# Kernel tuning notes

Hardware: AMD Instinct MI355X
Metric: run time of the kernel (lower is better)

The kernel has to match this reference:

```python
import jax, jax.numpy as jnp
import numpy as np

N, M_DIM, CTRL = 16384, 512, 1024
EPS = 1e-16

def setup_inputs() -> dict:
    key = jax.random.key(0)
    k1, k2, k3, k4, k5 = jax.random.split(key, 5)
    embeddings = jax.random.normal(k1, (1, CTRL), dtype=jnp.float32)
    w_prev = jax.random.uniform(k2, (1, N), dtype=jnp.float32)
    w_prev = w_prev / jnp.sum(w_prev, axis=1, keepdims=True)  # valid soft address
    memory = jax.random.normal(k3, (N, M_DIM), dtype=jnp.float32) * 0.05
    out_f = 3 * M_DIM + 6  # write_lengths = [M,1,1,3,1,M,M]
    W = jax.random.normal(k4, (out_f, CTRL), dtype=jnp.float32) * (1.0 / np.sqrt(CTRL))
    b = jax.random.normal(k5, (out_f,), dtype=jnp.float32) * 0.01
    return {"embeddings": embeddings, "w_prev": w_prev, "memory": memory, "W": W, "b": b}

def reference(embeddings, w_prev, memory, W, b):
    Md = memory.shape[1]
    o = (embeddings @ W.T + b).reshape(1, -1)  # [1, 3M+6]
    # column split per write_lengths [M,1,1,3,1,M,M]
    k = o[:, :Md]
    beta = jax.nn.softplus(o[:, Md:Md + 1])
    g = jax.nn.sigmoid(o[:, Md + 1:Md + 2])
    s = jax.nn.softmax(o[:, Md + 2:Md + 5], axis=1)       # 3 circular shifts
    gamma = 1.0 + jax.nn.softplus(o[:, Md + 5:Md + 6])
    e = o[:, Md + 6:2 * Md + 6]                            # erase vector [1,M]
    a = o[:, 2 * Md + 6:]                                  # add vector   [1,M]
    # content addressing: cosine similarity of k against each memory row
    mem_norm = jnp.linalg.norm(memory, axis=1)             # [N]
    k_norm = jnp.linalg.norm(k, axis=1)                    # [1]
    sim = (k @ memory.T) / (k_norm[:, None] * mem_norm[None, :] + EPS)  # [1,N]
    wc = jax.nn.softmax(beta * sim, axis=1)
    # interpolation with previous weights
    wg = g * wc + (1.0 - g) * w_prev
    # circular convolution with 3-tap shift kernel (shifts -1,0,+1)
    ws = (s[:, 0:1] * jnp.roll(wg, 1, axis=1)
          + s[:, 1:2] * wg
          + s[:, 2:3] * jnp.roll(wg, -1, axis=1))
    # sharpening
    wp = jnp.power(ws + EPS, gamma)
    w = wp / jnp.sum(wp, axis=1, keepdims=True)            # [1,N]
    # erase/add outer-product memory write
    erase = w.T @ e                                        # [N,M]
    add = w.T @ a                                          # [N,M]
    new_memory = memory * (1.0 - erase) + add
    return w, new_memory
```

## Files before the change

kernel.cpp:

```cpp
#include <hip/hip_runtime.h>
#include <math.h>

#define N 16384
#define MD 512
#define CTRLDIM 1024
#define OUTF 1542


__device__ __forceinline__ float softplus_f(float x) {
    return (x > 20.f) ? x : log1pf(expf(x));
}

__device__ __forceinline__ float wave_bfly_sum(float v) {
    #pragma unroll
    for (int off = 1; off < 64; off <<= 1) v += __shfl_xor(v, off, 64);
    return v;
}

__global__ void k_proj(const float* __restrict__ emb, const float* __restrict__ W,
                       const float* __restrict__ b, float* __restrict__ O,
                       float* __restrict__ E, float* __restrict__ A) {
    int row = blockIdx.x;
    int t = threadIdx.x;
    const float4* w4 = (const float4*)(W + (size_t)row * CTRLDIM);
    const float4* e4 = (const float4*)emb;
    float4 wv = w4[t];
    float4 ev = e4[t];
    float p = wv.x * ev.x + wv.y * ev.y + wv.z * ev.z + wv.w * ev.w;
    #pragma unroll
    for (int off = 32; off; off >>= 1) p += __shfl_down(p, off, 64);
    __shared__ float s[4];
    int lane = t & 63, wid = t >> 6;
    if (lane == 0) s[wid] = p;
    __syncthreads();
    if (t == 0) {
        float val = s[0] + s[1] + s[2] + s[3] + b[row];
        O[row] = val;
        if (row >= MD + 6 && row < 2 * MD + 6)      E[row - (MD + 6)] = val;
        else if (row >= 2 * MD + 6)                 A[row - (2 * MD + 6)] = val;
    }
}

__global__ void __launch_bounds__(256) k_sim(const float* __restrict__ mem,
                                             const float* __restrict__ O,
                                             float* __restrict__ EZ,
                                             float* __restrict__ PART1) {
    int t = threadIdx.x, lane = t & 63, wid = t >> 6;
    int waveId = blockIdx.x * 4 + wid;
    const float4* k4 = (const float4*)O;
    float4 k0 = k4[lane], k1 = k4[lane + 64];
    float ksq = k0.x * k0.x + k0.y * k0.y + k0.z * k0.z + k0.w * k0.w
              + k1.x * k1.x + k1.y * k1.y + k1.z * k1.z + k1.w * k1.w;
    ksq = wave_bfly_sum(ksq);
    float knorm = sqrtf(ksq);
    float beta = softplus_f(O[MD]);
    int row0 = waveId * 4;
    float4 m0[4], m1[4];
    #pragma unroll
    for (int r = 0; r < 4; r++) {
        const float4* m4 = (const float4*)(mem + (size_t)(row0 + r) * MD);
        m0[r] = m4[lane];
        m1[r] = m4[lane + 64];
    }
    float wsum = 0.f;
    #pragma unroll
    for (int r = 0; r < 4; r++) {
        float dot = m0[r].x * k0.x + m0[r].y * k0.y + m0[r].z * k0.z + m0[r].w * k0.w
                  + m1[r].x * k1.x + m1[r].y * k1.y + m1[r].z * k1.z + m1[r].w * k1.w;
        float nsq = m0[r].x * m0[r].x + m0[r].y * m0[r].y + m0[r].z * m0[r].z + m0[r].w * m0[r].w
                  + m1[r].x * m1[r].x + m1[r].y * m1[r].y + m1[r].z * m1[r].z + m1[r].w * m1[r].w;
        dot = wave_bfly_sum(dot);
        nsq = wave_bfly_sum(nsq);
        float z = beta * dot / (knorm * sqrtf(nsq) + 1e-16f);
        float ez = expf(z - beta);
        if (lane == 0) EZ[row0 + r] = ez;
        wsum += ez;
    }
    __shared__ float sblk[4];
    if (lane == 0) sblk[wid] = wsum;
    __syncthreads();
    if (t == 0) PART1[blockIdx.x] = sblk[0] + sblk[1] + sblk[2] + sblk[3];
}

__global__ void __launch_bounds__(256) k_shift(const float* __restrict__ EZ,
                                               const float* __restrict__ wprev,
                                               const float* __restrict__ O,
                                               const float* __restrict__ PART1,
                                               float* __restrict__ WP,
                                               float* __restrict__ PART2) {
    int t = threadIdx.x, lane = t & 63, wid = t >> 6;
    float v = 0.f;
    #pragma unroll
    for (int j = 0; j < 16; j++) v += PART1[lane + j * 64];
    float inv1 = 1.f / wave_bfly_sum(v);
    float g = 1.f / (1.f + expf(-O[MD + 1]));
    float s0r = O[MD + 2], s1r = O[MD + 3], s2r = O[MD + 4];
    float m = fmaxf(s0r, fmaxf(s1r, s2r));
    float e0 = expf(s0r - m), e1 = expf(s1r - m), e2 = expf(s2r - m);
    float inv_se = 1.f / (e0 + e1 + e2);
    float s0 = e0 * inv_se, s1 = e1 * inv_se, s2 = e2 * inv_se;
    float gamma = 1.f + softplus_f(O[MD + 5]);
    float gm1 = 1.f - g;
    int i = blockIdx.x * 256 + t;
    int im = (i == 0) ? (N - 1) : (i - 1);
    int ip = (i == N - 1) ? 0 : (i + 1);
    float wgm = g * EZ[im] * inv1 + gm1 * wprev[im];
    float wgc = g * EZ[i]  * inv1 + gm1 * wprev[i];
    float wgp = g * EZ[ip] * inv1 + gm1 * wprev[ip];
    float wsv = s0 * wgm + s1 * wgc + s2 * wgp;
    float wp = exp2f(gamma * log2f(wsv + 1e-16f));
    WP[i] = wp;
    float bs = wave_bfly_sum(wp);
    __shared__ float sblk[4];
    if (lane == 0) sblk[wid] = bs;
    __syncthreads();
    if (t == 0) PART2[blockIdx.x] = sblk[0] + sblk[1] + sblk[2] + sblk[3];
}

__global__ void __launch_bounds__(256) k_upd(const float* __restrict__ mem,
                                             const float* __restrict__ WP,
                                             const float* __restrict__ PART2,
                                             const float* __restrict__ E,
                                             const float* __restrict__ A,
                                             float* __restrict__ wout,
                                             float* __restrict__ outMem) {
    int t = threadIdx.x, lane = t & 63;
    float inv2 = 1.f / wave_bfly_sum(PART2[lane]);
    int idx = blockIdx.x * 256 + t;
    int i = idx >> 7;
    int c = idx & 127;
    float wi = WP[i] * inv2;
    if (c == 0) wout[i] = wi;
    float4 m = ((const float4*)mem)[idx];
    float4 e = ((const float4*)E)[c];
    float4 a = ((const float4*)A)[c];
    float4 o;
    o.x = m.x * (1.f - wi * e.x) + wi * a.x;
    o.y = m.y * (1.f - wi * e.y) + wi * a.y;
    o.z = m.z * (1.f - wi * e.z) + wi * a.z;
    o.w = m.w * (1.f - wi * e.w) + wi * a.w;
    ((float4*)outMem)[idx] = o;
}

extern "C" void kernel_launch(void* const* d_in, const int* in_sizes, int n_in,
                              void* d_out, int out_size, void* d_ws, size_t ws_size,
                              hipStream_t stream) {
    const float* emb   = (const float*)d_in[0];
    const float* wprev = (const float*)d_in[1];
    const float* mem   = (const float*)d_in[2];
    const float* W     = (const float*)d_in[3];
    const float* b     = (const float*)d_in[4];
    float* out = (float*)d_out;
    float* wsf = (float*)d_ws;
    float* O     = wsf;
    float* E     = wsf + 1552;
    float* A     = wsf + 2064;
    float* PART1 = wsf + 2576;
    float* PART2 = wsf + 3600;
    float* EZ    = wsf + 3664;
    float* WP    = wsf + 20048;

    k_proj<<<OUTF, 256, 0, stream>>>(emb, W, b, O, E, A);
    k_sim<<<N / 16, 256, 0, stream>>>(mem, O, EZ, PART1);
    k_shift<<<N / 256, 256, 0, stream>>>(EZ, wprev, O, PART1, WP, PART2);
    k_upd<<<(N * (MD / 4)) / 256, 256, 0, stream>>>(mem, WP, PART2, E, A, out, out + N);
}
```

Before: 110.9 us.

## Fuse four kernels into one cooperative persistent kernel with grid syncs

Replaces the four separate launches (projection, similarity, shift/sharpen, memory update) with a single cooperative kernel of 1024 blocks that uses grid.sync between phases. This removes three launch gaps and their inter-kernel drain. In exchange it adds grid-wide barrier cost and leaves most blocks idle during the shift phase. The update phase loops over a fixed grid instead of one element per thread.

```diff
diff --git a/kernel.cpp b/kernel.cpp
--- a/kernel.cpp
+++ b/kernel.cpp
@@ -1,10 +1,15 @@
 #include <hip/hip_runtime.h>
+#include <hip/hip_cooperative_groups.h>
 #include <math.h>
+
+namespace cg = cooperative_groups;
 
 #define N 16384
 #define MD 512
 #define CTRLDIM 1024
 #define OUTF 1542
+#define NBLK 1024
+#define NTHR 256
 
 
 __device__ __forceinline__ float softplus_f(float x) {
@@ -17,129 +22,133 @@
     return v;
 }
 
-__global__ void k_proj(const float* __restrict__ emb, const float* __restrict__ W,
-                       const float* __restrict__ b, float* __restrict__ O,
-                       float* __restrict__ E, float* __restrict__ A) {
-    int row = blockIdx.x;
-    int t = threadIdx.x;
-    const float4* w4 = (const float4*)(W + (size_t)row * CTRLDIM);
-    const float4* e4 = (const float4*)emb;
-    float4 wv = w4[t];
-    float4 ev = e4[t];
-    float p = wv.x * ev.x + wv.y * ev.y + wv.z * ev.z + wv.w * ev.w;
-    #pragma unroll
-    for (int off = 32; off; off >>= 1) p += __shfl_down(p, off, 64);
-    __shared__ float s[4];
-    int lane = t & 63, wid = t >> 6;
-    if (lane == 0) s[wid] = p;
-    __syncthreads();
-    if (t == 0) {
-        float val = s[0] + s[1] + s[2] + s[3] + b[row];
-        O[row] = val;
-        if (row >= MD + 6 && row < 2 * MD + 6)      E[row - (MD + 6)] = val;
-        else if (row >= 2 * MD + 6)                 A[row - (2 * MD + 6)] = val;
+__global__ void __launch_bounds__(NTHR, 4) k_fused(
+        const float* __restrict__ emb, const float* __restrict__ wprev,
+        const float* __restrict__ mem, const float* __restrict__ W,
+        const float* __restrict__ b, float* __restrict__ wout,
+        float* __restrict__ outMem, float* __restrict__ wsf) {
+    cg::grid_group grid = cg::this_grid();
+    float* O     = wsf;
+    float* E     = wsf + 1552;
+    float* A     = wsf + 2064;
+    float* PART1 = wsf + 2576;
+    float* PART2 = wsf + 3600;
+    float* EZ    = wsf + 3664;
+    float* WP    = wsf + 20048;
+
+    int t = threadIdx.x, lane = t & 63, wid = t >> 6;
+    __shared__ float sblk[4];
+
+    for (int row = blockIdx.x; row < OUTF; row += NBLK) {
+        const float4* w4 = (const float4*)(W + (size_t)row * CTRLDIM);
+        const float4* e4 = (const float4*)emb;
+        float4 wv = w4[t];
+        float4 ev = e4[t];
+        float p = wv.x * ev.x + wv.y * ev.y + wv.z * ev.z + wv.w * ev.w;
+        p = wave_bfly_sum(p);
+        if (lane == 0) sblk[wid] = p;
+        __syncthreads();
+        if (t == 0) {
+            float val = sblk[0] + sblk[1] + sblk[2] + sblk[3] + b[row];
+            O[row] = val;
+            if (row >= MD + 6 && row < 2 * MD + 6)  E[row - (MD + 6)] = val;
+            else if (row >= 2 * MD + 6)             A[row - (2 * MD + 6)] = val;
+        }
+        __syncthreads();
     }
-}
+    grid.sync();
 
-__global__ void __launch_bounds__(256) k_sim(const float* __restrict__ mem,
-                                             const float* __restrict__ O,
-                                             float* __restrict__ EZ,
-                                             float* __restrict__ PART1) {
-    int t = threadIdx.x, lane = t & 63, wid = t >> 6;
-    int waveId = blockIdx.x * 4 + wid;
-    const float4* k4 = (const float4*)O;
-    float4 k0 = k4[lane], k1 = k4[lane + 64];
-    float ksq = k0.x * k0.x + k0.y * k0.y + k0.z * k0.z + k0.w * k0.w
-              + k1.x * k1.x + k1.y * k1.y + k1.z * k1.z + k1.w * k1.w;
-    ksq = wave_bfly_sum(ksq);
-    float knorm = sqrtf(ksq);
-    float beta = softplus_f(O[MD]);
-    int row0 = waveId * 4;
-    float4 m0[4], m1[4];
-    #pragma unroll
-    for (int r = 0; r < 4; r++) {
-        const float4* m4 = (const float4*)(mem + (size_t)(row0 + r) * MD);
-        m0[r] = m4[lane];
-        m1[r] = m4[lane + 64];
+    {
+        const float4* k4 = (const float4*)O;
+        float4 k0 = k4[lane], k1 = k4[lane + 64];
+        float ksq = k0.x * k0.x + k0.y * k0.y + k0.z * k0.z + k0.w * k0.w
+                  + k1.x * k1.x + k1.y * k1.y + k1.z * k1.z + k1.w * k1.w;
+        ksq = wave_bfly_sum(ksq);
+        float knorm = sqrtf(ksq);
+        float beta = softplus_f(O[MD]);
+        int row0 = (blockIdx.x * 4 + wid) * 4;
+        float4 m0[4], m1[4];
+        #pragma unroll
+        for (int r = 0; r < 4; r++) {
+            const float4* m4 = (const float4*)(mem + (size_t)(row0 + r) * MD);
+            m0[r] = m4[lane];
+            m1[r] = m4[lane + 64];
+        }
+        float wsum = 0.f;
+        #pragma unroll
+        for (int r = 0; r < 4; r++) {
+            float dot = m0[r].x * k0.x + m0[r].y * k0.y + m0[r].z * k0.z + m0[r].w * k0.w
+                      + m1[r].x * k1.x + m1[r].y * k1.y + m1[r].z * k1.z + m1[r].w * k1.w;
+            float nsq = m0[r].x * m0[r].x + m0[r].y * m0[r].y + m0[r].z * m0[r].z + m0[r].w * m0[r].w
+                      + m1[r].x * m1[r].x + m1[r].y * m1[r].y + m1[r].z * m1[r].z + m1[r].w * m1[r].w;
+            dot = wave_bfly_sum(dot);
+            nsq = wave_bfly_sum(nsq);
+            float z = beta * dot / (knorm * sqrtf(nsq) + 1e-16f);
+            float ez = expf(z - beta);
+            if (lane == 0) EZ[row0 + r] = ez;
+            wsum += ez;
+        }
+        __syncthreads();
+        if (lane == 0) sblk[wid] = wsum;
+        __syncthreads();
+        if (t == 0) PART1[blockIdx.x] = sblk[0] + sblk[1] + sblk[2] + sblk[3];
     }
-    float wsum = 0.f;
-    #pragma unroll
-    for (int r = 0; r < 4; r++) {
-        float dot = m0[r].x * k0.x + m0[r].y * k0.y + m0[r].z * k0.z + m0[r].w * k0.w
-                  + m1[r].x * k1.x + m1[r].y * k1.y + m1[r].z * k1.z + m1[r].w * k1.w;
-        float nsq = m0[r].x * m0[r].x + m0[r].y * m0[r].y + m0[r].z * m0[r].z + m0[r].w * m0[r].w
-                  + m1[r].x * m1[r].x + m1[r].y * m1[r].y + m1[r].z * m1[r].z + m1[r].w * m1[r].w;
-        dot = wave_bfly_sum(dot);
-        nsq = wave_bfly_sum(nsq);
-        float z = beta * dot / (knorm * sqrtf(nsq) + 1e-16f);
-        float ez = expf(z - beta);
-        if (lane == 0) EZ[row0 + r] = ez;
-        wsum += ez;
+    grid.sync();
+
+    if (blockIdx.x < 64) {
+        float v = 0.f;
+        #pragma unroll
+        for (int j = 0; j < 16; j++) v += PART1[lane + j * 64];
+        float inv1 = 1.f / wave_bfly_sum(v);
+        float g = 1.f / (1.f + expf(-O[MD + 1]));
+        float s0r = O[MD + 2], s1r = O[MD + 3], s2r = O[MD + 4];
+        float m = fmaxf(s0r, fmaxf(s1r, s2r));
+        float e0 = expf(s0r - m), e1 = expf(s1r - m), e2 = expf(s2r - m);
+        float inv_se = 1.f / (e0 + e1 + e2);
+        float s0 = e0 * inv_se, s1 = e1 * inv_se, s2 = e2 * inv_se;
+        float gamma = 1.f + softplus_f(O[MD + 5]);
+        float gm1 = 1.f - g;
+        int i = blockIdx.x * 256 + t;
+        int im = (i == 0) ? (N - 1) : (i - 1);
+        int ip = (i == N - 1) ? 0 : (i + 1);
+        float wgm = g * EZ[im] * inv1 + gm1 * wprev[im];
+        float wgc = g * EZ[i]  * inv1 + gm1 * wprev[i];
+        float wgp = g * EZ[ip] * inv1 + gm1 * wprev[ip];
+        float wsv = s0 * wgm + s1 * wgc + s2 * wgp;
+        float wp = exp2f(gamma * log2f(wsv + 1e-16f));
+        WP[i] = wp;
+        float bs = wave_bfly_sum(wp);
+        __syncthreads();
+        if (lane == 0) sblk[wid] = bs;
+        __syncthreads();
+        if (t == 0) PART2[blockIdx.x] = sblk[0] + sblk[1] + sblk[2] + sblk[3];
     }
-    __shared__ float sblk[4];
-    if (lane == 0) sblk[wid] = wsum;
-    __syncthreads();
-    if (t == 0) PART1[blockIdx.x] = sblk[0] + sblk[1] + sblk[2] + sblk[3];
-}
+    grid.sync();
 
-__global__ void __launch_bounds__(256) k_shift(const float* __restrict__ EZ,
-                                               const float* __restrict__ wprev,
-                                               const float* __restrict__ O,
-                                               const float* __restrict__ PART1,
-                                               float* __restrict__ WP,
-                                               float* __restrict__ PART2) {
-    int t = threadIdx.x, lane = t & 63, wid = t >> 6;
-    float v = 0.f;
-    #pragma unroll
-    for (int j = 0; j < 16; j++) v += PART1[lane + j * 64];
-    float inv1 = 1.f / wave_bfly_sum(v);
-    float g = 1.f / (1.f + expf(-O[MD + 1]));
-    float s0r = O[MD + 2], s1r = O[MD + 3], s2r = O[MD + 4];
-    float m = fmaxf(s0r, fmaxf(s1r, s2r));
-    float e0 = expf(s0r - m), e1 = expf(s1r - m), e2 = expf(s2r - m);
-    float inv_se = 1.f / (e0 + e1 + e2);
-    float s0 = e0 * inv_se, s1 = e1 * inv_se, s2 = e2 * inv_se;
-    float gamma = 1.f + softplus_f(O[MD + 5]);
-    float gm1 = 1.f - g;
-    int i = blockIdx.x * 256 + t;
-    int im = (i == 0) ? (N - 1) : (i - 1);
-    int ip = (i == N - 1) ? 0 : (i + 1);
-    float wgm = g * EZ[im] * inv1 + gm1 * wprev[im];
-    float wgc = g * EZ[i]  * inv1 + gm1 * wprev[i];
-    float wgp = g * EZ[ip] * inv1 + gm1 * wprev[ip];
-    float wsv = s0 * wgm + s1 * wgc + s2 * wgp;
-    float wp = exp2f(gamma * log2f(wsv + 1e-16f));
-    WP[i] = wp;
-    float bs = wave_bfly_sum(wp);
-    __shared__ float sblk[4];
-    if (lane == 0) sblk[wid] = bs;
-    __syncthreads();
-    if (t == 0) PART2[blockIdx.x] = sblk[0] + sblk[1] + sblk[2] + sblk[3];
-}
-
-__global__ void __launch_bounds__(256) k_upd(const float* __restrict__ mem,
-                                             const float* __restrict__ WP,
-                                             const float* __restrict__ PART2,
-                                             const float* __restrict__ E,
-                                             const float* __restrict__ A,
-                                             float* __restrict__ wout,
-                                             float* __restrict__ outMem) {
-    int t = threadIdx.x, lane = t & 63;
-    float inv2 = 1.f / wave_bfly_sum(PART2[lane]);
-    int idx = blockIdx.x * 256 + t;
-    int i = idx >> 7;
-    int c = idx & 127;
-    float wi = WP[i] * inv2;
-    if (c == 0) wout[i] = wi;
-    float4 m = ((const float4*)mem)[idx];
-    float4 e = ((const float4*)E)[c];
-    float4 a = ((const float4*)A)[c];
-    float4 o;
-    o.x = m.x * (1.f - wi * e.x) + wi * a.x;
-    o.y = m.y * (1.f - wi * e.y) + wi * a.y;
-    o.z = m.z * (1.f - wi * e.z) + wi * a.z;
-    o.w = m.w * (1.f - wi * e.w) + wi * a.w;
-    ((float4*)outMem)[idx] = o;
+    {
+        float inv2 = 1.f / wave_bfly_sum(PART2[lane]);
+        const float4* m4 = (const float4*)mem;
+        const float4* e4 = (const float4*)E;
+        const float4* a4 = (const float4*)A;
+        float4* o4 = (float4*)outMem;
+        #pragma unroll
+        for (int it = 0; it < (N * (MD / 4)) / (NBLK * NTHR); it++) {
+            int idx = it * (NBLK * NTHR) + blockIdx.x * NTHR + t;
+            int i = idx >> 7;
+            int c = idx & 127;
+            float wi = WP[i] * inv2;
+            if (c == 0) wout[i] = wi;
+            float4 mv = m4[idx];
+            float4 e = e4[c];
+            float4 a = a4[c];
+            float4 o;
+            o.x = mv.x * (1.f - wi * e.x) + wi * a.x;
+            o.y = mv.y * (1.f - wi * e.y) + wi * a.y;
+            o.z = mv.z * (1.f - wi * e.z) + wi * a.z;
+            o.w = mv.w * (1.f - wi * e.w) + wi * a.w;
+            o4[idx] = o;
+        }
+    }
 }
 
 extern "C" void kernel_launch(void* const* d_in, const int* in_sizes, int n_in,
@@ -150,18 +159,12 @@
     const float* mem   = (const float*)d_in[2];
     const float* W     = (const float*)d_in[3];
     const float* b     = (const float*)d_in[4];
-    float* out = (float*)d_out;
-    float* wsf = (float*)d_ws;
-    float* O     = wsf;
-    float* E     = wsf + 1552;
-    float* A     = wsf + 2064;
-    float* PART1 = wsf + 2576;
-    float* PART2 = wsf + 3600;
-    float* EZ    = wsf + 3664;
-    float* WP    = wsf + 20048;
+    float* wout   = (float*)d_out;
+    float* outMem = wout + N;
+    float* wsf    = (float*)d_ws;
 
-    k_proj<<<OUTF, 256, 0, stream>>>(emb, W, b, O, E, A);
-    k_sim<<<N / 16, 256, 0, stream>>>(mem, O, EZ, PART1);
-    k_shift<<<N / 256, 256, 0, stream>>>(EZ, wprev, O, PART1, WP, PART2);
-    k_upd<<<(N * (MD / 4)) / 256, 256, 0, stream>>>(mem, WP, PART2, E, A, out, out + N);
+    void* args[] = {(void*)&emb, (void*)&wprev, (void*)&mem, (void*)&W,
+                    (void*)&b, (void*)&wout, (void*)&outMem, (void*)&wsf};
+    hipLaunchCooperativeKernel((void*)k_fused, dim3(NBLK), dim3(NTHR),
+                               args, 0, stream);
 }
```

New measurement: 385.1 us. +247.1%, slower.
